# Kernel optimization log

Hardware: AMD Instinct MI355X
Metric: run time of the kernel (lower is better)

The kernel has to match this reference:

```python
import jax, jax.numpy as jnp
import numpy as np

EMBED_DIM = 768
NUM_HEADS = 12
HEAD_DIM = EMBED_DIM // NUM_HEADS


def setup_inputs() -> dict:
    key = jax.random.key(0)
    k_x, k_wqkv, k_bqkv, k_wp, k_bp = jax.random.split(key, 5)
    B, N, C = 2, 2048, EMBED_DIM
    lim_qkv = 1.0 / np.sqrt(C)
    lim_p = 1.0 / np.sqrt(C)
    return {
        "x": jax.random.normal(k_x, (B, N, C), dtype=jnp.float32),
        # torch Linear weights: [out_features, in_features]
        "w_qkv": jax.random.uniform(k_wqkv, (3 * C, C), minval=-lim_qkv, maxval=lim_qkv, dtype=jnp.float32),
        "b_qkv": jax.random.uniform(k_bqkv, (3 * C,), minval=-lim_qkv, maxval=lim_qkv, dtype=jnp.float32),
        "w_proj": jax.random.uniform(k_wp, (C, C), minval=-lim_p, maxval=lim_p, dtype=jnp.float32),
        "b_proj": jax.random.uniform(k_bp, (C,), minval=-lim_p, maxval=lim_p, dtype=jnp.float32),
    }


def reference(x, w_qkv, b_qkv, w_proj, b_proj):
    b, n, c = x.shape
    h, d = NUM_HEADS, HEAD_DIM
    qkv = x @ w_qkv.T + b_qkv                      # [b, n, 3c]
    qkv = qkv.reshape(b, n, 3, h, d).transpose(2, 0, 3, 1, 4)  # [3, b, h, n, d]
    q, k, v = qkv[0], qkv[1], qkv[2]
    scale = d ** -0.5
    attn = jnp.einsum('bhnd,bhmd->bhnm', q, k) * scale  # [b, h, n, n]
    attn = jax.nn.softmax(attn, axis=-1)
    # dropout is identity at inference (eval mode)
    out = jnp.einsum('bhnm,bhmd->bhnd', attn, v)        # [b, h, n, d]
    out = out.transpose(0, 2, 1, 3).reshape(b, n, c)    # [b, n, c]
    return out @ w_proj.T + b_proj
```

## Files before the change

### kernel.cpp

```cpp
#include <hip/hip_runtime.h>
#include <cstdint>
#include <cstddef>

using u16    = uint16_t;
using u16x4  = __attribute__((ext_vector_type(4))) uint16_t;
using u16x8  = __attribute__((ext_vector_type(8))) uint16_t;
using bf16x2 = __attribute__((ext_vector_type(2))) __bf16;
using bf16x8 = __attribute__((ext_vector_type(8))) __bf16;
using f32x4  = __attribute__((ext_vector_type(4))) float;
using f32x16 = __attribute__((ext_vector_type(16))) float;

__device__ __forceinline__ u16 f2b(float f) {
    union { float f; uint32_t u; } x; x.f = f;
    uint32_t r = x.u + 0x7FFFu + ((x.u >> 16) & 1u);
    return (u16)(r >> 16);
}
__device__ __forceinline__ uint32_t pk2(float a, float b) {
    bf16x2 t; t[0] = (__bf16)a; t[1] = (__bf16)b;
    return __builtin_bit_cast(uint32_t, t);
}
__device__ __forceinline__ bf16x8 ld8(const u16* p) {
    union { u16x8 v; u16x4 h[2]; } r;
    r.h[0] = *(const u16x4*)p;
    r.h[1] = *(const u16x4*)(p + 4);
    return __builtin_bit_cast(bf16x8, r.v);
}
__device__ __forceinline__ u16x8 ld8u(const u16* p) {
    union { u16x8 v; u16x4 h[2]; } r;
    r.h[0] = *(const u16x4*)p;
    r.h[1] = *(const u16x4*)(p + 4);
    return r.v;
}
__device__ __forceinline__ bf16x8 ldvf(const u16* p) {
    union { u16x8 v; u16x4 h[2]; } r;
    r.h[0] = *(const u16x4*)p;
    r.h[1] = *(const u16x4*)(p + 8);
    return __builtin_bit_cast(bf16x8, r.v);
}
__device__ __forceinline__ void st8(u16* p, u16x8 v) {
    union { u16x8 v; u16x4 h[2]; } r; r.v = v;
    *(u16x4*)p       = r.h[0];
    *(u16x4*)(p + 4) = r.h[1];
}

__device__ __forceinline__ void load16_async(const u16* g, u16* lds_base) {
    __builtin_amdgcn_global_load_lds(
        (const __attribute__((address_space(1))) u16*)g,
        (__attribute__((address_space(3))) u16*)(uint32_t)(uintptr_t)lds_base,
        16, 0, 0);
}

__global__ void conv_k(const float* __restrict__ x,  u16* __restrict__ xb,  int nx4,
                       const float* __restrict__ w1, u16* __restrict__ w1b, int n14,
                       const float* __restrict__ w2, u16* __restrict__ w2b, int n24)
{
    const int t   = blockIdx.x * blockDim.x + threadIdx.x;
    const int stp = gridDim.x * blockDim.x;
    for (int i = t; i < nx4; i += stp) {
        f32x4 v = ((const f32x4*)x)[i];
        u16x4 o;
        #pragma unroll
        for (int e = 0; e < 4; e++) o[e] = f2b(v[e]);
        ((u16x4*)xb)[i] = o;
    }
    for (int i = t; i < n14; i += stp) {
        f32x4 v = ((const f32x4*)w1)[i];
        u16x4 o;
        #pragma unroll
        for (int e = 0; e < 4; e++) o[e] = f2b(v[e]);
        ((u16x4*)w1b)[i] = o;
    }
    for (int i = t; i < n24; i += stp) {
        f32x4 v = ((const f32x4*)w2)[i];
        u16x4 o;
        #pragma unroll
        for (int e = 0; e < 4; e++) o[e] = f2b(v[e]);
        ((u16x4*)w2b)[i] = o;
    }
}

__global__ __launch_bounds__(256, 3) void gemm_qkv(
    const u16* __restrict__ A, const u16* __restrict__ W,
    const float* __restrict__ bias,
    u16* __restrict__ O0, u16* __restrict__ O1, u16* __restrict__ O2)
{
    __shared__ alignas(16) char smem[33792];
    u16* As = (u16*)smem;
    u16* Bs = (u16*)(smem + 8192);
    u16* T  = (u16*)smem;

    const int tid  = threadIdx.x;
    const int wid  = tid >> 6, lane = tid & 63;
    const int quad = lane >> 4, lc = lane & 15;
    const int row0 = blockIdx.x * 128, col0 = blockIdx.y * 128;
    const int wm   = (wid >> 1) * 64, wn = (wid & 1) * 64;

    const int srA = wid * 32 + (lane >> 2);
    const int scA = (lane & 3) * 8;

    f32x4 acc[4][4] = {};

    for (int k0 = 0; k0 < 768; k0 += 32) {
        __syncthreads();
        #pragma unroll
        for (int t = 0; t < 2; t++) {
            load16_async(&A[(row0 + srA + t*16) * 768 + k0 + scA], &As[wid*1024 + t*512]);
            load16_async(&W[(col0 + srA + t*16) * 768 + k0 + scA], &Bs[wid*1024 + t*512]);
        }
        __syncthreads();

        bf16x8 a[4], b[4];
        #pragma unroll
        for (int i = 0; i < 4; i++)
            a[i] = __builtin_bit_cast(bf16x8, *(const u16x8*)&As[(wm + i*16 + lc)*32 + quad*8]);
        #pragma unroll
        for (int j = 0; j < 4; j++)
            b[j] = __builtin_bit_cast(bf16x8, *(const u16x8*)&Bs[(wn + j*16 + lc)*32 + quad*8]);
        #pragma unroll
        for (int i = 0; i < 4; i++)
            #pragma unroll
            for (int j = 0; j < 4; j++)
                acc[i][j] = __builtin_amdgcn_mfma_f32_16x16x32_bf16(a[i], b[j], acc[i][j], 0, 0, 0);
    }

    if (col0 < 1536) {
        #pragma unroll
        for (int i = 0; i < 4; i++) {
            #pragma unroll
            for (int j = 0; j < 4; j++) {
                const int gc = col0 + wn + j*16 + lc;
                const float bv = bias[gc];
                #pragma unroll
                for (int r = 0; r < 4; r++) {
                    const int gr = row0 + wm + i*16 + quad*4 + r;
                    const u16 ob = f2b(acc[i][j][r] + bv);
                    if (gc < 768) O0[gr * 768 + gc] = ob;
                    else          O1[gr * 768 + (gc - 768)] = ob;
                }
            }
        }
    } else {
        __syncthreads();
        #pragma unroll
        for (int j = 0; j < 4; j++) {
            const int cl = wn + j*16 + lc;
            const float bv = bias[col0 + cl];
            #pragma unroll
            for (int i = 0; i < 4; i++) {
                uint2 w;
                w.x = pk2(acc[i][j][0] + bv, acc[i][j][1] + bv);
                w.y = pk2(acc[i][j][2] + bv, acc[i][j][3] + bv);
                *(uint2*)&T[cl*132 + wm + i*16 + quad*4] = w;
            }
        }
        __syncthreads();

        const int cl = tid >> 1;
        const int sg = (tid & 1) * 64;
        const int c2 = (col0 - 1536) + cl;
        const int hh = c2 >> 6, dd = c2 & 63;
        const int bb = row0 >> 11, nn0 = row0 & 2047;
        u16* dst = &O2[((size_t)((bb*12 + hh)*64 + dd))*2048 + nn0 + sg];
        #pragma unroll
        for (int k = 0; k < 8; k++)
            *(u16x8*)&dst[k*8] = ld8u(&T[cl*132 + sg + k*8]);
    }
}

__global__ __launch_bounds__(256, 4) void gemm_proj(
    const u16* __restrict__ A, const u16* __restrict__ W,
    const float* __restrict__ bias, float* __restrict__ F0)
{
    __shared__ alignas(16) u16 As[64 * 32];
    __shared__ alignas(16) u16 Bs[64 * 32];
    const int tid  = threadIdx.x;
    const int wid  = tid >> 6, lane = tid & 63;
    const int quad = lane >> 4, lc = lane & 15;
    const int row0 = blockIdx.x * 64, col0 = blockIdx.y * 64;
    const int wm   = (wid >> 1) * 32, wn = (wid & 1) * 32;

    const int srA = wid * 16 + (lane >> 2);
    const int scA = (lane & 3) * 8;

    f32x4 acc[2][2] = {};

    for (int k0 = 0; k0 < 768; k0 += 32) {
        __syncthreads();
        load16_async(&A[(row0 + srA) * 768 + k0 + scA], &As[wid*512]);
        load16_async(&W[(col0 + srA) * 768 + k0 + scA], &Bs[wid*512]);
        __syncthreads();

        bf16x8 a[2], b[2];
        #pragma unroll
        for (int i = 0; i < 2; i++)
            a[i] = __builtin_bit_cast(bf16x8, *(const u16x8*)&As[(wm + i*16 + lc)*32 + quad*8]);
        #pragma unroll
        for (int j = 0; j < 2; j++)
            b[j] = __builtin_bit_cast(bf16x8, *(const u16x8*)&Bs[(wn + j*16 + lc)*32 + quad*8]);
        #pragma unroll
        for (int i = 0; i < 2; i++)
            #pragma unroll
            for (int j = 0; j < 2; j++)
                acc[i][j] = __builtin_amdgcn_mfma_f32_16x16x32_bf16(a[i], b[j], acc[i][j], 0, 0, 0);
    }

    #pragma unroll
    for (int i = 0; i < 2; i++)
        #pragma unroll
        for (int j = 0; j < 2; j++) {
            const int gc = col0 + wn + j*16 + lc;
            const float bv = bias[gc];
            #pragma unroll
            for (int r = 0; r < 4; r++) {
                const int gr = row0 + wm + i*16 + quad*4 + r;
                F0[gr * 768 + gc] = acc[i][j][r] + bv;
            }
        }
}

__global__ __launch_bounds__(256, 4) void attn_k(
    const u16* __restrict__ Q, const u16* __restrict__ K,
    const u16* __restrict__ V, u16* __restrict__ O)
{
    __shared__ alignas(16) char lds[35328];
    u16* Ks = (u16*)(lds);
    u16* Vs = (u16*)(lds + 17408);
    float* Obuf = (float*)(lds);
    float* Lbuf = (float*)(lds + 33792);

    const int tid  = threadIdx.x;
    const int wid  = tid >> 6, lane = tid & 63;
    const int hl   = lane >> 5;
    const int lr   = lane & 31;
    const int li = blockIdx.x;
    const int bh = li >> 6, qt = li & 63;
    const int b = bh / 12, h = bh - b * 12;
    const int q0 = qt * 32;

    const u16* Qp = Q + ((size_t)b * 2048) * 768 + h * 64;
    const u16* Kp = K + ((size_t)b * 2048) * 768 + h * 64;
    const u16* Vp = V + (size_t)bh * 64 * 2048;
    u16*       Op = O + ((size_t)b * 2048) * 768 + h * 64;

    bf16x8 qf[4];
    #pragma unroll
    for (int c = 0; c < 4; c++) {
        u16x8 t = *(const u16x8*)&Qp[(q0 + lr) * 768 + c*16 + hl*8];
        bf16x8 sc;
        #pragma unroll
        for (int e = 0; e < 8; e++) {
            union { uint32_t u; float f; } z; z.u = ((uint32_t)t[e]) << 16;
            sc[e] = (__bf16)(z.f * 0.125f);
        }
        qf[c] = sc;
    }

    float l_ = 0.f;
    f32x16 o0 = {}, o1 = {};

    const int kr = tid >> 3, kseg = (tid & 7) * 8;
    const int vr = tid >> 4, vseg = (tid & 15) * 8;
    const int kb0 = wid * 32;

    u16x8 kpre[4], vpre[4];
    #pragma unroll
    for (int p = 0; p < 4; p++)
        kpre[p] = *(const u16x8*)&Kp[(kr + p*32)*768 + kseg];
    #pragma unroll
    for (int p = 0; p < 4; p++)
        vpre[p] = *(const u16x8*)&Vp[(vr + p*16)*2048 + vseg];

    for (int kt = 0; kt < 16; kt++) {
        __syncthreads();
        #pragma unroll
        for (int p = 0; p < 4; p++)
            st8(&Ks[(kr + p*32)*68 + kseg], kpre[p]);
        #pragma unroll
        for (int p = 0; p < 4; p++)
            st8(&Vs[(vr + p*16)*140 + vseg], vpre[p]);
        __syncthreads();

        if (kt < 15) {
            #pragma unroll
            for (int p = 0; p < 4; p++)
                kpre[p] = *(const u16x8*)&Kp[((kt+1)*128 + kr + p*32)*768 + kseg];
            #pragma unroll
            for (int p = 0; p < 4; p++)
                vpre[p] = *(const u16x8*)&Vp[(vr + p*16)*2048 + (kt+1)*128 + vseg];
        }

        f32x16 s = {};
        __builtin_amdgcn_s_setprio(1);
        #pragma unroll
        for (int c = 0; c < 4; c++) {
            bf16x8 kf = ld8(&Ks[(kb0 + lr)*68 + c*16 + hl*8]);
            s = __builtin_amdgcn_mfma_f32_32x32x16_bf16(kf, qf[c], s, 0, 0, 0);
        }
        __builtin_amdgcn_s_setprio(0);

        #pragma unroll
        for (int r = 0; r < 16; r++) {
            float p = __expf(s[r]);
            s[r] = p;
            l_ += p;
        }

        union { bf16x8 v; uint32_t w[4]; } pb0, pb1;
        #pragma unroll
        for (int e2 = 0; e2 < 4; e2++) {
            pb0.w[e2] = pk2(s[2*e2],     s[2*e2 + 1]);
            pb1.w[e2] = pk2(s[8 + 2*e2], s[8 + 2*e2 + 1]);
        }

        const int v4 = kb0 + hl*4;
        {
            bf16x8 va0 = ldvf(&Vs[(0*32 + lr)*140 + v4]);
            bf16x8 va1 = ldvf(&Vs[(0*32 + lr)*140 + v4 + 16]);
            bf16x8 vb0 = ldvf(&Vs[(1*32 + lr)*140 + v4]);
            bf16x8 vb1 = ldvf(&Vs[(1*32 + lr)*140 + v4 + 16]);
            __builtin_amdgcn_s_setprio(1);
            o0 = __builtin_amdgcn_mfma_f32_32x32x16_bf16(va0, pb0.v, o0, 0, 0, 0);
            o0 = __builtin_amdgcn_mfma_f32_32x32x16_bf16(va1, pb1.v, o0, 0, 0, 0);
            o1 = __builtin_amdgcn_mfma_f32_32x32x16_bf16(vb0, pb0.v, o1, 0, 0, 0);
            o1 = __builtin_amdgcn_mfma_f32_32x32x16_bf16(vb1, pb1.v, o1, 0, 0, 0);
            __builtin_amdgcn_s_setprio(0);
        }
    }

    l_ += __shfl_xor(l_, 32);
    __syncthreads();
    if (lane < 32)
        Lbuf[wid*32 + lr] = l_;

    #pragma unroll
    for (int r = 0; r < 16; r++) {
        const int dr = (r & 3) + 8*(r >> 2) + 4*hl;
        Obuf[(wid*64 + dr)*33 + lr]      = o0[r];
        Obuf[(wid*64 + 32 + dr)*33 + lr] = o1[r];
    }
    __syncthreads();

    const int q  = tid & 31;
    const int dblk = tid >> 5;
    const float linv = 1.0f / (Lbuf[q] + Lbuf[32 + q] + Lbuf[64 + q] + Lbuf[96 + q]);

    u16x8 ov;
    #pragma unroll
    for (int j = 0; j < 8; j++) {
        const int d = dblk*8 + j;
        const float sum = Obuf[(0*64 + d)*33 + q] + Obuf[(1*64 + d)*33 + q] +
                          Obuf[(2*64 + d)*33 + q] + Obuf[(3*64 + d)*33 + q];
        ov[j] = f2b(sum * linv);
    }
    *(u16x8*)&Op[(size_t)(q0 + q) * 768 + dblk*8] = ov;
}

extern "C" void kernel_launch(void* const* d_in, const int* in_sizes, int n_in,
                              void* d_out, int out_size, void* d_ws, size_t ws_size,
                              hipStream_t stream)
{
    const float* x    = (const float*)d_in[0];
    const float* wqkv = (const float*)d_in[1];
    const float* bqkv = (const float*)d_in[2];
    const float* wp   = (const float*)d_in[3];
    const float* bp   = (const float*)d_in[4];
    float* out = (float*)d_out;
    char* ws = (char*)d_ws;

    u16* Qw    = (u16*)(ws);
    u16* Vt    = (u16*)(ws + 6291456);
    u16* wqkvb = (u16*)(ws + 12582912);
    u16* wpb   = (u16*)(ws + 16121856);
    u16* Kw    = (u16*)d_out;
    u16* xb    = (u16*)((char*)d_out + 6291456);

    conv_k<<<512, 256, 0, stream>>>(x, xb, 3145728/4, wqkv, wqkvb, 1769472/4, wp, wpb, 589824/4);
    gemm_qkv<<<dim3(32, 18), 256, 0, stream>>>(xb, wqkvb, bqkv, Qw, Kw, Vt);
    attn_k<<<1536, 256, 0, stream>>>(Qw, Kw, Vt, Qw);
    gemm_proj<<<dim3(64, 12), 256, 0, stream>>>(Qw, wpb, bp, out);
}
```

Measured before the change: 159.4 us.

## Load K/V fragments directly to registers and process 64 queries per attention block

```diff
diff --git a/kernel.cpp b/kernel.cpp
--- a/kernel.cpp
+++ b/kernel.cpp
@@ -19,28 +19,18 @@
     bf16x2 t; t[0] = (__bf16)a; t[1] = (__bf16)b;
     return __builtin_bit_cast(uint32_t, t);
 }
-__device__ __forceinline__ bf16x8 ld8(const u16* p) {
-    union { u16x8 v; u16x4 h[2]; } r;
-    r.h[0] = *(const u16x4*)p;
-    r.h[1] = *(const u16x4*)(p + 4);
-    return __builtin_bit_cast(bf16x8, r.v);
-}
 __device__ __forceinline__ u16x8 ld8u(const u16* p) {
     union { u16x8 v; u16x4 h[2]; } r;
     r.h[0] = *(const u16x4*)p;
     r.h[1] = *(const u16x4*)(p + 4);
     return r.v;
 }
-__device__ __forceinline__ bf16x8 ldvf(const u16* p) {
-    union { u16x8 v; u16x4 h[2]; } r;
-    r.h[0] = *(const u16x4*)p;
-    r.h[1] = *(const u16x4*)(p + 8);
-    return __builtin_bit_cast(bf16x8, r.v);
-}
-__device__ __forceinline__ void st8(u16* p, u16x8 v) {
-    union { u16x8 v; u16x4 h[2]; } r; r.v = v;
-    *(u16x4*)p       = r.h[0];
-    *(u16x4*)(p + 4) = r.h[1];
+__device__ __forceinline__ float ex2(float x) {
+#if __has_builtin(__builtin_amdgcn_exp2f)
+    return __builtin_amdgcn_exp2f(x);
+#else
+    return __expf(x * 0.6931471805599453f);
+#endif
 }
 
 __device__ __forceinline__ void load16_async(const u16* g, u16* lds_base) {
@@ -161,9 +151,17 @@
         const int hh = c2 >> 6, dd = c2 & 63;
         const int bb = row0 >> 11, nn0 = row0 & 2047;
         u16* dst = &O2[((size_t)((bb*12 + hh)*64 + dd))*2048 + nn0 + sg];
-        #pragma unroll
-        for (int k = 0; k < 8; k++)
-            *(u16x8*)&dst[k*8] = ld8u(&T[cl*132 + sg + k*8]);
+        const u16* src = &T[cl*132 + sg];
+        #pragma unroll
+        for (int g = 0; g < 2; g++)
+            #pragma unroll
+            for (int sub = 0; sub < 4; sub++) {
+                const int off = g*32 + (sub & 1)*4 + (sub >> 1)*16;
+                union { u16x8 v; u16x4 h[2]; } r;
+                r.h[0] = *(const u16x4*)&src[off];
+                r.h[1] = *(const u16x4*)&src[off + 8];
+                *(u16x8*)&dst[g*32 + sub*8] = r.v;
+            }
     }
 }
 
@@ -218,14 +216,12 @@
         }
 }
 
-__global__ __launch_bounds__(256, 4) void attn_k(
+__global__ __launch_bounds__(256, 3) void attn_k(
     const u16* __restrict__ Q, const u16* __restrict__ K,
     const u16* __restrict__ V, u16* __restrict__ O)
 {
-    __shared__ alignas(16) char lds[35328];
-    u16* Ks = (u16*)(lds);
-    u16* Vs = (u16*)(lds + 17408);
-    float* Obuf = (float*)(lds);
+    __shared__ alignas(16) char lds[34304];
+    float* Obuf = (float*)lds;
     float* Lbuf = (float*)(lds + 33792);
 
     const int tid  = threadIdx.x;
@@ -233,126 +229,155 @@
     const int hl   = lane >> 5;
     const int lr   = lane & 31;
     const int li = blockIdx.x;
-    const int bh = li >> 6, qt = li & 63;
+    const int bh = li >> 5, qt = li & 31;
     const int b = bh / 12, h = bh - b * 12;
-    const int q0 = qt * 32;
+    const int q0 = qt * 64;
 
     const u16* Qp = Q + ((size_t)b * 2048) * 768 + h * 64;
     const u16* Kp = K + ((size_t)b * 2048) * 768 + h * 64;
     const u16* Vp = V + (size_t)bh * 64 * 2048;
     u16*       Op = O + ((size_t)b * 2048) * 768 + h * 64;
 
-    bf16x8 qf[4];
+    const float qs = 0.125f * 1.4426950408889634f;
+    bf16x8 qf[2][4];
     #pragma unroll
-    for (int c = 0; c < 4; c++) {
-        u16x8 t = *(const u16x8*)&Qp[(q0 + lr) * 768 + c*16 + hl*8];
-        bf16x8 sc;
-        #pragma unroll
-        for (int e = 0; e < 8; e++) {
-            union { uint32_t u; float f; } z; z.u = ((uint32_t)t[e]) << 16;
-            sc[e] = (__bf16)(z.f * 0.125f);
-        }
-        qf[c] = sc;
-    }
-
-    float l_ = 0.f;
-    f32x16 o0 = {}, o1 = {};
-
-    const int kr = tid >> 3, kseg = (tid & 7) * 8;
-    const int vr = tid >> 4, vseg = (tid & 15) * 8;
+    for (int qh = 0; qh < 2; qh++)
+        #pragma unroll
+        for (int c = 0; c < 4; c++) {
+            u16x8 t = *(const u16x8*)&Qp[(q0 + qh*32 + lr) * 768 + c*16 + hl*8];
+            bf16x8 sc;
+            #pragma unroll
+            for (int e = 0; e < 8; e++) {
+                union { uint32_t u; float f; } z; z.u = ((uint32_t)t[e]) << 16;
+                sc[e] = (__bf16)(z.f * qs);
+            }
+            qf[qh][c] = sc;
+        }
+
+    float l0 = 0.f, l1 = 0.f;
+    f32x16 o00 = {}, o01 = {}, o10 = {}, o11 = {};
+
     const int kb0 = wid * 32;
-
-    u16x8 kpre[4], vpre[4];
+    const u16* Krow = &Kp[(kb0 + lr) * 768 + hl*8];
+    const u16* Vr0  = &Vp[(size_t)lr * 2048 + kb0 + hl*8];
+    const u16* Vr1  = Vr0 + 32 * 2048;
+
+    bf16x8 kreg[4];
     #pragma unroll
-    for (int p = 0; p < 4; p++)
-        kpre[p] = *(const u16x8*)&Kp[(kr + p*32)*768 + kseg];
-    #pragma unroll
-    for (int p = 0; p < 4; p++)
-        vpre[p] = *(const u16x8*)&Vp[(vr + p*16)*2048 + vseg];
+    for (int c = 0; c < 4; c++)
+        kreg[c] = __builtin_bit_cast(bf16x8, *(const u16x8*)&Krow[c*16]);
 
     for (int kt = 0; kt < 16; kt++) {
-        __syncthreads();
-        #pragma unroll
-        for (int p = 0; p < 4; p++)
-            st8(&Ks[(kr + p*32)*68 + kseg], kpre[p]);
-        #pragma unroll
-        for (int p = 0; p < 4; p++)
-            st8(&Vs[(vr + p*16)*140 + vseg], vpre[p]);
-        __syncthreads();
+        const int koff = kt * 128;
+        bf16x8 va0 = __builtin_bit_cast(bf16x8, *(const u16x8*)&Vr0[koff]);
+        bf16x8 va1 = __builtin_bit_cast(bf16x8, *(const u16x8*)&Vr0[koff + 16]);
+        bf16x8 vb0 = __builtin_bit_cast(bf16x8, *(const u16x8*)&Vr1[koff]);
+        bf16x8 vb1 = __builtin_bit_cast(bf16x8, *(const u16x8*)&Vr1[koff + 16]);
+
+        f32x16 s0 = {}, s1 = {};
+        __builtin_amdgcn_s_setprio(1);
+        #pragma unroll
+        for (int c = 0; c < 4; c++)
+            s0 = __builtin_amdgcn_mfma_f32_32x32x16_bf16(kreg[c], qf[0][c], s0, 0, 0, 0);
+        #pragma unroll
+        for (int c = 0; c < 4; c++)
+            s1 = __builtin_amdgcn_mfma_f32_32x32x16_bf16(kreg[c], qf[1][c], s1, 0, 0, 0);
+        __builtin_amdgcn_s_setprio(0);
 
         if (kt < 15) {
-            #pragma unroll
-            for (int p = 0; p < 4; p++)
-                kpre[p] = *(const u16x8*)&Kp[((kt+1)*128 + kr + p*32)*768 + kseg];
-            #pragma unroll
-            for (int p = 0; p < 4; p++)
-                vpre[p] = *(const u16x8*)&Vp[(vr + p*16)*2048 + (kt+1)*128 + vseg];
-        }
-
-        f32x16 s = {};
+            const int kn = koff * 768 + 98304;
+            #pragma unroll
+            for (int c = 0; c < 4; c++)
+                kreg[c] = __builtin_bit_cast(bf16x8, *(const u16x8*)&Krow[kn + c*16]);
+        }
+
+        #pragma unroll
+        for (int r = 0; r < 16; r++) {
+            float p = ex2(s0[r]);
+            s0[r] = p;
+            l0 += p;
+        }
+        union { bf16x8 v; uint32_t w[4]; } p00, p01;
+        #pragma unroll
+        for (int e2 = 0; e2 < 4; e2++) {
+            p00.w[e2] = pk2(s0[2*e2],     s0[2*e2 + 1]);
+            p01.w[e2] = pk2(s0[8 + 2*e2], s0[8 + 2*e2 + 1]);
+        }
         __builtin_amdgcn_s_setprio(1);
-        #pragma unroll
-        for (int c = 0; c < 4; c++) {
-            bf16x8 kf = ld8(&Ks[(kb0 + lr)*68 + c*16 + hl*8]);
-            s = __builtin_amdgcn_mfma_f32_32x32x16_bf16(kf, qf[c], s, 0, 0, 0);
-        }
+        o00 = __builtin_amdgcn_mfma_f32_32x32x16_bf16(va0, p00.v, o00, 0, 0, 0);
+        o00 = __builtin_amdgcn_mfma_f32_32x32x16_bf16(va1, p01.v, o00, 0, 0, 0);
+        o01 = __builtin_amdgcn_mfma_f32_32x32x16_bf16(vb0, p00.v, o01, 0, 0, 0);
+        o01 = __builtin_amdgcn_mfma_f32_32x32x16_bf16(vb1, p01.v, o01, 0, 0, 0);
         __builtin_amdgcn_s_setprio(0);
 
         #pragma unroll
         for (int r = 0; r < 16; r++) {
-            float p = __expf(s[r]);
-            s[r] = p;
-            l_ += p;
-        }
-
-        union { bf16x8 v; uint32_t w[4]; } pb0, pb1;
+            float p = ex2(s1[r]);
+            s1[r] = p;
+            l1 += p;
+        }
+        union { bf16x8 v; uint32_t w[4]; } p10, p11;
         #pragma unroll
         for (int e2 = 0; e2 < 4; e2++) {
-            pb0.w[e2] = pk2(s[2*e2],     s[2*e2 + 1]);
-            pb1.w[e2] = pk2(s[8 + 2*e2], s[8 + 2*e2 + 1]);
-        }
-
-        const int v4 = kb0 + hl*4;
-        {
-            bf16x8 va0 = ldvf(&Vs[(0*32 + lr)*140 + v4]);
-            bf16x8 va1 = ldvf(&Vs[(0*32 + lr)*140 + v4 + 16]);
-            bf16x8 vb0 = ldvf(&Vs[(1*32 + lr)*140 + v4]);
-            bf16x8 vb1 = ldvf(&Vs[(1*32 + lr)*140 + v4 + 16]);
-            __builtin_amdgcn_s_setprio(1);
-            o0 = __builtin_amdgcn_mfma_f32_32x32x16_bf16(va0, pb0.v, o0, 0, 0, 0);
-            o0 = __builtin_amdgcn_mfma_f32_32x32x16_bf16(va1, pb1.v, o0, 0, 0, 0);
-            o1 = __builtin_amdgcn_mfma_f32_32x32x16_bf16(vb0, pb0.v, o1, 0, 0, 0);
-            o1 = __builtin_amdgcn_mfma_f32_32x32x16_bf16(vb1, pb1.v, o1, 0, 0, 0);
-            __builtin_amdgcn_s_setprio(0);
-        }
-    }
-
-    l_ += __shfl_xor(l_, 32);
-    __syncthreads();
-    if (lane < 32)
-        Lbuf[wid*32 + lr] = l_;
-
+            p10.w[e2] = pk2(s1[2*e2],     s1[2*e2 + 1]);
+            p11.w[e2] = pk2(s1[8 + 2*e2], s1[8 + 2*e2 + 1]);
+        }
+        __builtin_amdgcn_s_setprio(1);
+        o10 = __builtin_amdgcn_mfma_f32_32x32x16_bf16(va0, p10.v, o10, 0, 0, 0);
+        o10 = __builtin_amdgcn_mfma_f32_32x32x16_bf16(va1, p11.v, o10, 0, 0, 0);
+        o11 = __builtin_amdgcn_mfma_f32_32x32x16_bf16(vb0, p10.v, o11, 0, 0, 0);
+        o11 = __builtin_amdgcn_mfma_f32_32x32x16_bf16(vb1, p11.v, o11, 0, 0, 0);
+        __builtin_amdgcn_s_setprio(0);
+    }
+
+    l0 += __shfl_xor(l0, 32);
+    l1 += __shfl_xor(l1, 32);
+
+    const int q  = tid & 31;
+    const int dblk = tid >> 5;
+
+    if (lane < 32) Lbuf[wid*32 + lr] = l0;
     #pragma unroll
     for (int r = 0; r < 16; r++) {
         const int dr = (r & 3) + 8*(r >> 2) + 4*hl;
-        Obuf[(wid*64 + dr)*33 + lr]      = o0[r];
-        Obuf[(wid*64 + 32 + dr)*33 + lr] = o1[r];
+        Obuf[(wid*64 + dr)*33 + lr]      = o00[r];
+        Obuf[(wid*64 + 32 + dr)*33 + lr] = o01[r];
     }
     __syncthreads();
-
-    const int q  = tid & 31;
-    const int dblk = tid >> 5;
-    const float linv = 1.0f / (Lbuf[q] + Lbuf[32 + q] + Lbuf[64 + q] + Lbuf[96 + q]);
-
-    u16x8 ov;
+    {
+        const float linv = 1.0f / (Lbuf[q] + Lbuf[32 + q] + Lbuf[64 + q] + Lbuf[96 + q]);
+        u16x8 ov;
+        #pragma unroll
+        for (int j = 0; j < 8; j++) {
+            const int d = dblk*8 + j;
+            const float sum = Obuf[(0*64 + d)*33 + q] + Obuf[(1*64 + d)*33 + q] +
+                              Obuf[(2*64 + d)*33 + q] + Obuf[(3*64 + d)*33 + q];
+            ov[j] = f2b(sum * linv);
+        }
+        *(u16x8*)&Op[(size_t)(q0 + q) * 768 + dblk*8] = ov;
+    }
+    __syncthreads();
+
+    if (lane < 32) Lbuf[wid*32 + lr] = l1;
     #pragma unroll
-    for (int j = 0; j < 8; j++) {
-        const int d = dblk*8 + j;
-        const float sum = Obuf[(0*64 + d)*33 + q] + Obuf[(1*64 + d)*33 + q] +
-                          Obuf[(2*64 + d)*33 + q] + Obuf[(3*64 + d)*33 + q];
-        ov[j] = f2b(sum * linv);
-    }
-    *(u16x8*)&Op[(size_t)(q0 + q) * 768 + dblk*8] = ov;
+    for (int r = 0; r < 16; r++) {
+        const int dr = (r & 3) + 8*(r >> 2) + 4*hl;
+        Obuf[(wid*64 + dr)*33 + lr]      = o10[r];
+        Obuf[(wid*64 + 32 + dr)*33 + lr] = o11[r];
+    }
+    __syncthreads();
+    {
+        const float linv = 1.0f / (Lbuf[q] + Lbuf[32 + q] + Lbuf[64 + q] + Lbuf[96 + q]);
+        u16x8 ov;
+        #pragma unroll
+        for (int j = 0; j < 8; j++) {
+            const int d = dblk*8 + j;
+            const float sum = Obuf[(0*64 + d)*33 + q] + Obuf[(1*64 + d)*33 + q] +
+                              Obuf[(2*64 + d)*33 + q] + Obuf[(3*64 + d)*33 + q];
+            ov[j] = f2b(sum * linv);
+        }
+        *(u16x8*)&Op[(size_t)(q0 + 32 + q) * 768 + dblk*8] = ov;
+    }
 }
 
 extern "C" void kernel_launch(void* const* d_in, const int* in_sizes, int n_in,
@@ -376,6 +401,6 @@
 
     conv_k<<<512, 256, 0, stream>>>(x, xb, 3145728/4, wqkv, wqkvb, 1769472/4, wp, wpb, 589824/4);
     gemm_qkv<<<dim3(32, 18), 256, 0, stream>>>(xb, wqkvb, bqkv, Qw, Kw, Vt);
-    attn_k<<<1536, 256, 0, stream>>>(Qw, Kw, Vt, Qw);
+    attn_k<<<768, 256, 0, stream>>>(Qw, Kw, Vt, Qw);
     gemm_proj<<<dim3(64, 12), 256, 0, stream>>>(Qw, wpb, bp, out);
 }
```

New measurement: 192.4 us. 1.21x slower.
